# Kernel tuning notes

Measured on AMD Instinct MI355X. Metric: run time of the kernel, lower is better.

## Reference

```python
import jax, jax.numpy as jnp
import numpy as np

D_MODEL = 1024
NUM_HEADS = 16
DEPTH = D_MODEL // NUM_HEADS
MAX_LEN = 5000
B, S = 4, 1024


def _dense(x, W, b):
    return x @ W + b


def _split_heads(x, n_heads, depth):
    # [..., S, D] -> [..., H, S, depth]
    *lead, s, d = x.shape
    x = x.reshape(*lead, s, n_heads, depth)
    return jnp.swapaxes(x, -3, -2)


def setup_inputs() -> dict:
    key = jax.random.key(0)
    ks = jax.random.split(key, 12)
    w = 0.02  # glorot-ish scale to keep softmax logits sane
    inp = {
        'q': jax.random.normal(ks[0], (B, S, D_MODEL), jnp.float32),
        'k': jax.random.normal(ks[1], (B, S, D_MODEL), jnp.float32),
        'v': jax.random.normal(ks[2], (B, S, D_MODEL), jnp.float32),
        'Wq': jax.random.normal(ks[3], (D_MODEL, D_MODEL), jnp.float32) * w,
        'bq': jnp.zeros((D_MODEL,), jnp.float32),
        'Wk': jax.random.normal(ks[4], (D_MODEL, D_MODEL), jnp.float32) * w,
        'bk': jnp.zeros((D_MODEL,), jnp.float32),
        'Wv': jax.random.normal(ks[5], (D_MODEL, D_MODEL), jnp.float32) * w,
        'bv': jnp.zeros((D_MODEL,), jnp.float32),
        'Uq': jax.random.normal(ks[6], (D_MODEL, D_MODEL), jnp.float32) * w,
        'buq': jnp.zeros((D_MODEL,), jnp.float32),
        'Uk': jax.random.normal(ks[7], (D_MODEL, D_MODEL), jnp.float32) * w,
        'buk': jnp.zeros((D_MODEL,), jnp.float32),
        'pos_table': jax.random.normal(ks[8], (MAX_LEN, D_MODEL), jnp.float32) * w,
        'theta_cc': jnp.zeros((1, NUM_HEADS, 1, 1), jnp.float32),
        'theta_co': jnp.zeros((1, NUM_HEADS, 1, 1), jnp.float32),
        'theta_oc': jnp.zeros((1, NUM_HEADS, 1, 1), jnp.float32),
        'Wo': jax.random.normal(ks[9], (D_MODEL, D_MODEL), jnp.float32) * w,
        'bo': jnp.zeros((D_MODEL,), jnp.float32),
    }
    return inp


def reference(q, k, v, Wq, bq, Wk, bk, Wv, bv, Uq, buq, Uk, buk,
              pos_table, theta_cc, theta_co, theta_oc, Wo, bo):
    b, s, d = q.shape
    # content projections -> [B,H,S,depth]
    q_c = _split_heads(_dense(q, Wq, bq), NUM_HEADS, DEPTH)
    k_c = _split_heads(_dense(k, Wk, bk), NUM_HEADS, DEPTH)
    v_c = _split_heads(_dense(v, Wv, bv), NUM_HEADS, DEPTH)
    content_scores = jnp.einsum('bhqd,bhkd->bhqk', q_c, k_c)

    # untied positional scores (shared across batch): [1,H,S,S]
    pos_emb = pos_table[:s]                               # [S,D]
    q_p = _split_heads(_dense(pos_emb, Uq, buq)[None], NUM_HEADS, DEPTH)
    k_p = _split_heads(_dense(pos_emb, Uk, buk)[None], NUM_HEADS, DEPTH)
    pos_scores = jnp.einsum('bhqd,bhkd->bhqk', q_p, k_p)  # [1,H,S,S]

    # CLS-row/col overrides with learnable thetas
    pos_scores = pos_scores.at[:, :, 1:, 0:1].set(jnp.broadcast_to(theta_oc, (1, NUM_HEADS, s - 1, 1)))
    pos_scores = pos_scores.at[:, :, 0:1, 1:].set(jnp.broadcast_to(theta_co, (1, NUM_HEADS, 1, s - 1)))
    pos_scores = pos_scores.at[:, :, 0:1, 0:1].set(theta_cc)

    scores = (content_scores + pos_scores) / jnp.sqrt(jnp.float32(DEPTH))
    attn = jax.nn.softmax(scores, axis=-1)
    out = jnp.einsum('bhqk,bhkd->bhqd', attn, v_c)        # [B,H,S,depth]
    out = jnp.swapaxes(out, 1, 2).reshape(b, s, d)        # [B,S,D]
    return _dense(out, Wo, bo)
```

## Files before the change

kernel.cpp:

```cpp
#include <hip/hip_runtime.h>
#include <hip/hip_bf16.h>

typedef __hip_bfloat16 bf16;
typedef unsigned short u16;
typedef __attribute__((ext_vector_type(8))) short short8;
typedef __attribute__((ext_vector_type(4))) float f32x4;

#define D_MODEL 1024
#define NUM_HEADS 16
#define DEPTH 64
#define BATCH 4
#define SEQ 1024
#define BS (BATCH * SEQ)

__device__ __forceinline__ float ldDyn(const void* p, size_t i, int isbf) {
  return isbf ? __bfloat162float(((const bf16*)p)[i]) : ((const float*)p)[i];
}
__device__ __forceinline__ u16 f2bf(float f) {
  bf16 h = __float2bfloat16(f);
  return *(u16*)&h;
}
__device__ __forceinline__ void gl2lds16(const void* g, void* l) {
  __builtin_amdgcn_global_load_lds((const __attribute__((address_space(1))) unsigned int*)g,
                                   (__attribute__((address_space(3))) unsigned int*)l, 16, 0, 0);
}

__global__ void detect_kernel(const u16* __restrict__ q, int* __restrict__ flag) {
  if (threadIdx.x == 0 && blockIdx.x == 0) {
    int sane = 0;
    for (int i = 0; i < 64; ++i) {
      u16 h = q[2 * i];
      int e = (h >> 7) & 0xFF;
      if (e >= 100 && e <= 150) ++sane;
    }
    *flag = (sane >= 48) ? 1 : 0;
  }
}

__global__ __launch_bounds__(256) void convert_in(
    const void* __restrict__ q, const void* __restrict__ k, const void* __restrict__ v,
    const void* __restrict__ pos, u16* __restrict__ Qb, u16* __restrict__ Kb,
    u16* __restrict__ Vb, u16* __restrict__ Pb, const int* __restrict__ flagp) {
  const int isbf = *flagp;
  const int z = blockIdx.z;
  const void* src = (z == 0) ? q : (z == 1) ? k : (z == 2) ? v : pos;
  u16* dst = (z == 0) ? Qb : (z == 1) ? Kb : (z == 2) ? Vb : Pb;
  const size_t n8 = ((z == 3) ? (size_t)SEQ * D_MODEL : (size_t)BS * D_MODEL) / 8;
  for (size_t i = (size_t)blockIdx.x * 256 + threadIdx.x; i < n8; i += (size_t)gridDim.x * 256) {
    short8 o;
    if (isbf) {
      o = ((const short8*)src)[i];
    } else {
      const float4* f = (const float4*)src + 2 * i;
      float4 lo = f[0], hi = f[1];
      u16* pv = (u16*)&o;
      pv[0] = f2bf(lo.x); pv[1] = f2bf(lo.y); pv[2] = f2bf(lo.z); pv[3] = f2bf(lo.w);
      pv[4] = f2bf(hi.x); pv[5] = f2bf(hi.y); pv[6] = f2bf(hi.z); pv[7] = f2bf(hi.w);
    }
    ((short8*)dst)[i] = o;
  }
}

__global__ __launch_bounds__(256) void transpose_w(
    const void* W0, const void* W1, const void* W2, const void* W3, const void* W4,
    const void* W5, u16* __restrict__ WT, const int* __restrict__ flagp) {
  const int isbf = *flagp;
  const int z = blockIdx.z;
  const void* W = (z == 0) ? W0 : (z == 1) ? W1 : (z == 2) ? W2
                 : (z == 3) ? W3 : (z == 4) ? W4 : W5;
  u16* out = WT + (size_t)z * D_MODEL * D_MODEL;
  __shared__ u16 tile[32][33];
  const int t = threadIdx.x;
  const int tx = t & 31, ty = t >> 5;
  const int r0 = blockIdx.y * 32, c0 = blockIdx.x * 32;
#pragma unroll
  for (int i = 0; i < 4; ++i) {
    size_t gi = (size_t)(r0 + ty + 8 * i) * D_MODEL + c0 + tx;
    tile[ty + 8 * i][tx] = isbf ? ((const u16*)W)[gi] : f2bf(((const float*)W)[gi]);
  }
  __syncthreads();
#pragma unroll
  for (int i = 0; i < 4; ++i)
    out[(size_t)(c0 + ty + 8 * i) * D_MODEL + r0 + tx] = tile[tx][ty + 8 * i];
}

struct GArgs {
  const u16* A[5];
  const u16* W[5];
  const void* bias[5];
  void* C[5];
  int Mr[5];
  int om[5];
};

__global__ __launch_bounds__(256) void gemm_mfma(GArgs ga, const int* __restrict__ flagp) {
  const int isbf = *flagp;
  const int z = blockIdx.z;
  const int M = ga.Mr[z];
  const int lin = blockIdx.x + 8 * blockIdx.y;
  const int xcd = lin & 7;
  const int loc = lin >> 3;
  const int rowb = (loc & 3) * 8 + xcd;
  const int colb = loc >> 2;
  const int row0 = rowb * 128, col0 = colb * 128;
  if (row0 >= M) return;
  const u16* A = ga.A[z];
  const u16* WT = ga.W[z];
  const void* bias = ga.bias[z];
  void* C = ga.C[z];
  const int omode = ga.om[z];

  __shared__ short As[2][128][32];
  __shared__ short Bs[2][128][32];
  const int t = threadIdx.x;
  const int wave = t >> 6, lane = t & 63;
  const int quad = lane >> 4, c16 = lane & 15;
  const int wrow = wave >> 1, wcol = wave & 1;

  f32x4 acc[4][4];
#pragma unroll
  for (int mt = 0; mt < 4; ++mt)
#pragma unroll
    for (int nt = 0; nt < 4; ++nt) acc[mt][nt] = {0.f, 0.f, 0.f, 0.f};

#define G_STAGE(K0, BUF)                                                                  \
  {                                                                                       \
    _Pragma("unroll") for (int i = 0; i < 2; ++i) {                                       \
      int L = t + 256 * i;                                                                \
      int r = L >> 2;                                                                     \
      int kc = (L & 3) ^ ((r + (r >> 2)) & 3);                                            \
      gl2lds16(WT + (size_t)(col0 + r) * 1024 + (K0) + kc * 8,                            \
               (char*)&Bs[BUF][0][0] + (size_t)(i * 256 + wave * 64) * 16);               \
      gl2lds16(A + (size_t)(row0 + r) * 1024 + (K0) + kc * 8,                             \
               (char*)&As[BUF][0][0] + (size_t)(i * 256 + wave * 64) * 16);               \
    }                                                                                     \
  }

  G_STAGE(0, 0);
  __syncthreads();

  const int fsw = (c16 + (c16 >> 2)) & 3;

  for (int kk = 0; kk < 32; ++kk) {
    const int cur = kk & 1;
    if (kk < 31) G_STAGE((kk + 1) * 32, cur ^ 1);

    short8 af[4], bfv[4];
#pragma unroll
    for (int mt = 0; mt < 4; ++mt)
      af[mt] = *(const short8*)&As[cur][wrow * 64 + mt * 16 + c16][((quad ^ fsw) * 8)];
#pragma unroll
    for (int nt = 0; nt < 4; ++nt)
      bfv[nt] = *(const short8*)&Bs[cur][wcol * 64 + nt * 16 + c16][((quad ^ fsw) * 8)];
#pragma unroll
    for (int nt = 0; nt < 4; ++nt)
#pragma unroll
      for (int mt = 0; mt < 4; ++mt)
        acc[mt][nt] = __builtin_amdgcn_mfma_f32_16x16x32_bf16(af[mt], bfv[nt], acc[mt][nt], 0, 0, 0);

    __syncthreads();
  }
#undef G_STAGE

#pragma unroll
  for (int nt = 0; nt < 4; ++nt) {
    int gc = col0 + wcol * 64 + nt * 16 + c16;
    float bb = ldDyn(bias, gc, isbf);
#pragma unroll
    for (int mt = 0; mt < 4; ++mt) {
      int gr0 = row0 + wrow * 64 + mt * 16 + quad * 4;
      if (omode == 2) {
        __attribute__((ext_vector_type(4))) short pk;
#pragma unroll
        for (int r = 0; r < 4; ++r) pk[r] = (short)f2bf(acc[mt][nt][r] + bb);
        *(__attribute__((ext_vector_type(4))) short*)&((u16*)C)[(size_t)gc * M + gr0] = pk;
      } else if (omode == 1 || isbf) {
#pragma unroll
        for (int r = 0; r < 4; ++r)
          ((bf16*)C)[(size_t)(gr0 + r) * 1024 + gc] = __float2bfloat16(acc[mt][nt][r] + bb);
      } else {
#pragma unroll
        for (int r = 0; r < 4; ++r)
          ((float*)C)[(size_t)(gr0 + r) * 1024 + gc] = acc[mt][nt][r] + bb;
      }
    }
  }
}

__global__ __launch_bounds__(256) void flash_attn(
    const bf16* __restrict__ Qc, const bf16* __restrict__ Kc, const bf16* __restrict__ VcT,
    const bf16* __restrict__ Qp, const bf16* __restrict__ Kp,
    const void* __restrict__ th_cc, const void* __restrict__ th_co,
    const void* __restrict__ th_oc, bf16* __restrict__ O, const int* __restrict__ flagp) {
  const int isbf = *flagp;
  const int h = blockIdx.x, b = blockIdx.y, qt = blockIdx.z;
  const int t = threadIdx.x, wave = t >> 6, lane = t & 63;
  const int quad = lane >> 4, c16 = lane & 15;

  __shared__ short Kt[2][64][128];
  __shared__ short Vt[2][64][64];
  __shared__ short Pt[4][16][64];

  const float tcc = ldDyn(th_cc, h, isbf);
  const float tco = ldDyn(th_co, h, isbf);
  const float toc = ldDyn(th_oc, h, isbf);

  const bf16* kcb = Kc + (size_t)b * SEQ * 1024 + h * 64;
  const bf16* kpb = Kp + h * 64;
  const bf16* vtb = VcT + (size_t)(h * 64) * BS + (size_t)b * SEQ;

  const int rwK = lane >> 4, kcK = lane & 15;
  const int rwV = lane >> 3, kcV = lane & 7;

#define STAGE_K(KT2, BUF)                                                              \
  {                                                                                    \
    _Pragma("unroll") for (int i = 0; i < 4; ++i) {                                    \
      int r = wave * 16 + i * 4 + rwK;                                                 \
      int c = kcK ^ (r & 15);                                                          \
      int key = (KT2)*64 + r;                                                          \
      const bf16* src = (c < 8) ? kcb + (size_t)key * 1024 + c * 8                     \
                                : kpb + (size_t)key * 1024 + c * 8 - 64;               \
      gl2lds16(src, &Kt[BUF][wave * 16 + i * 4][0]);                                   \
    }                                                                                  \
  }
#define STAGE_V(KT2, BUF)                                                              \
  {                                                                                    \
    _Pragma("unroll") for (int j = 0; j < 2; ++j) {                                    \
      int d = wave * 16 + j * 8 + rwV;                                                 \
      int c = kcV ^ (d & 7);                                                           \
      gl2lds16(vtb + (size_t)d * BS + (KT2)*64 + c * 8, &Vt[BUF][wave * 16 + j * 8][0]); \
    }                                                                                  \
  }

  short8 qf[2][4];
#pragma unroll
  for (int mt = 0; mt < 2; ++mt) {
    int qrow = qt * 128 + wave * 32 + mt * 16 + c16;
#pragma unroll
    for (int ks = 0; ks < 4; ++ks) {
      int d = ks * 32 + quad * 8;
      const bf16* src = (d < 64) ? Qc + ((size_t)(b * SEQ + qrow)) * 1024 + h * 64 + d
                                 : Qp + (size_t)qrow * 1024 + h * 64 + (d - 64);
      qf[mt][ks] = *(const short8*)src;
    }
    if (qrow == 0) {
      qf[mt][2] = (short8)0;
      qf[mt][3] = (short8)0;
    }
  }

  f32x4 accO[2][4];
#pragma unroll
  for (int mt = 0; mt < 2; ++mt)
#pragma unroll
    for (int nt = 0; nt < 4; ++nt) accO[mt][nt] = {0.f, 0.f, 0.f, 0.f};
  float lrow[2][4] = {{0.f, 0.f, 0.f, 0.f}, {0.f, 0.f, 0.f, 0.f}};

  STAGE_K(0, 0);
  STAGE_V(0, 0);
  __syncthreads();
  if (t < 8) *(short8*)&Kt[0][0][64 + t * 8] = (short8)0;
  __syncthreads();

  for (int kt = 0; kt < 16; ++kt) {
    const int cur = kt & 1, nxt = cur ^ 1;
    if (kt < 15) {
      STAGE_K(kt + 1, nxt);
      STAGE_V(kt + 1, nxt);
    }

    f32x4 accS[2][4];
#pragma unroll
    for (int mt = 0; mt < 2; ++mt)
#pragma unroll
      for (int nt = 0; nt < 4; ++nt) accS[mt][nt] = {0.f, 0.f, 0.f, 0.f};
#pragma unroll
    for (int nt = 0; nt < 4; ++nt)
#pragma unroll
      for (int ks = 0; ks < 4; ++ks) {
        short8 kf = *(const short8*)&Kt[cur][nt * 16 + c16][((ks * 4 + quad) ^ c16) * 8];
#pragma unroll
        for (int mt = 0; mt < 2; ++mt)
          accS[mt][nt] = __builtin_amdgcn_mfma_f32_16x16x32_bf16(qf[mt][ks], kf, accS[mt][nt], 0, 0, 0);
      }

    short8 vbreg[2][4];
#pragma unroll
    for (int ks2 = 0; ks2 < 2; ++ks2)
#pragma unroll
      for (int nt = 0; nt < 4; ++nt)
        vbreg[ks2][nt] =
            *(const short8*)&Vt[cur][nt * 16 + c16][(((ks2 * 4 + quad) ^ (c16 & 7)) & 7) * 8];

#pragma unroll
    for (int mt = 0; mt < 2; ++mt) {
      float s[4][4];
#pragma unroll
      for (int nt = 0; nt < 4; ++nt)
#pragma unroll
        for (int r = 0; r < 4; ++r) s[nt][r] = accS[mt][nt][r] * 0.125f;

      if (kt == 0 || (qt == 0 && wave == 0 && mt == 0)) {
#pragma unroll
        for (int nt = 0; nt < 4; ++nt)
#pragma unroll
          for (int r = 0; r < 4; ++r) {
            int kcol = kt * 64 + nt * 16 + c16;
            int qrow = qt * 128 + wave * 32 + mt * 16 + quad * 4 + r;
            float add = 0.f;
            if (qrow == 0 && kcol == 0) add = tcc;
            else if (qrow == 0) add = tco;
            else if (kcol == 0) add = toc;
            s[nt][r] += add * 0.125f;
          }
      }
#pragma unroll
      for (int nt = 0; nt < 4; ++nt)
#pragma unroll
        for (int r = 0; r < 4; ++r) {
          float p = __expf(s[nt][r]);
          lrow[mt][r] += p;
          int row = quad * 4 + r;
          int ch = nt * 2 + (c16 >> 3);
          Pt[wave][row][((ch ^ (row & 7)) * 8) + (c16 & 7)] = (short)f2bf(p);
        }
#pragma unroll
      for (int ks2 = 0; ks2 < 2; ++ks2) {
        short8 pf = *(const short8*)&Pt[wave][c16][(((ks2 * 4 + quad) ^ (c16 & 7)) & 7) * 8];
#pragma unroll
        for (int nt = 0; nt < 4; ++nt)
          accO[mt][nt] = __builtin_amdgcn_mfma_f32_16x16x32_bf16(pf, vbreg[ks2][nt], accO[mt][nt], 0, 0, 0);
      }
    }
    __syncthreads();
  }

#pragma unroll
  for (int d = 1; d < 16; d <<= 1)
#pragma unroll
    for (int mt = 0; mt < 2; ++mt)
#pragma unroll
      for (int r = 0; r < 4; ++r) lrow[mt][r] += __shfl_xor(lrow[mt][r], d, 64);

#pragma unroll
  for (int mt = 0; mt < 2; ++mt)
#pragma unroll
    for (int nt = 0; nt < 4; ++nt)
#pragma unroll
      for (int r = 0; r < 4; ++r) {
        int qrow = qt * 128 + wave * 32 + mt * 16 + quad * 4 + r;
        O[((size_t)(b * SEQ + qrow)) * 1024 + h * 64 + nt * 16 + c16] =
            __float2bfloat16(accO[mt][nt][r] / lrow[mt][r]);
      }
#undef STAGE_K
#undef STAGE_V
}

extern "C" void kernel_launch(void* const* d_in, const int* in_sizes, int n_in,
                              void* d_out, int out_size, void* d_ws, size_t ws_size,
                              hipStream_t stream) {
  const void* q = d_in[0];
  const void* k = d_in[1];
  const void* v = d_in[2];
  const void* Wq = d_in[3];
  const void* bq = d_in[4];
  const void* Wk = d_in[5];
  const void* bk = d_in[6];
  const void* Wv = d_in[7];
  const void* bv = d_in[8];
  const void* Uq = d_in[9];
  const void* buq = d_in[10];
  const void* Uk = d_in[11];
  const void* buk = d_in[12];
  const void* pos = d_in[13];
  const void* th_cc = d_in[14];
  const void* th_co = d_in[15];
  const void* th_oc = d_in[16];
  const void* Wo = d_in[17];
  const void* bo = d_in[18];

  const int M = BS;
  const size_t DD = (size_t)D_MODEL * D_MODEL;
  char* wsb = (char*)d_ws;
  int* flag = (int*)wsb;
  bf16* Qc = (bf16*)(wsb + 256);
  bf16* Kc = Qc + (size_t)M * D_MODEL;
  bf16* VcT = Kc + (size_t)M * D_MODEL;
  bf16* Qp = VcT + (size_t)M * D_MODEL;
  bf16* Kp = Qp + (size_t)SEQ * D_MODEL;
  u16* WT = (u16*)(Kp + (size_t)SEQ * D_MODEL);
  bf16* AO = (bf16*)WT;
  u16* Qb = WT + 6 * DD;
  u16* Kb = Qb + (size_t)M * D_MODEL;
  u16* Vb = Kb + (size_t)M * D_MODEL;
  u16* Pb = Vb + (size_t)M * D_MODEL;

  detect_kernel<<<1, 64, 0, stream>>>((const u16*)q, flag);

  dim3 blk(256);
  convert_in<<<dim3(512, 1, 4), blk, 0, stream>>>(q, k, v, pos, Qb, Kb, Vb, Pb, flag);
  transpose_w<<<dim3(32, 32, 6), blk, 0, stream>>>(Wq, Wk, Wv, Uq, Uk, Wo, WT, flag);

  GArgs g1 = {{Qb, Kb, Vb, Pb, Pb},
              {WT + 0 * DD, WT + 1 * DD, WT + 2 * DD, WT + 3 * DD, WT + 4 * DD},
              {bq, bk, bv, buq, buk},
              {Qc, Kc, VcT, Qp, Kp},
              {M, M, M, SEQ, SEQ},
              {1, 1, 2, 1, 1}};
  gemm_mfma<<<dim3(8, 32, 5), blk, 0, stream>>>(g1, flag);

  flash_attn<<<dim3(NUM_HEADS, BATCH, SEQ / 128), blk, 0, stream>>>(
      Qc, Kc, VcT, Qp, Kp, th_cc, th_co, th_oc, AO, flag);

  GArgs g2 = {{(const u16*)AO, (const u16*)AO, (const u16*)AO, (const u16*)AO, (const u16*)AO},
              {WT + 5 * DD, WT + 5 * DD, WT + 5 * DD, WT + 5 * DD, WT + 5 * DD},
              {bo, bo, bo, bo, bo},
              {d_out, d_out, d_out, d_out, d_out},
              {M, M, M, M, M},
              {0, 0, 0, 0, 0}};
  gemm_mfma<<<dim3(8, 32, 1), blk, 0, stream>>>(g2, flag);
}
```

Baseline: 291.3 us.

## Triple-buffer GEMM K-loop with vmcnt waits and prioritize MFMA in attention

Converts the projection GEMM from a double-buffered loop with a full __syncthreads per K step to a three-stage ring buffer. It prefetches two stages ahead and uses s_waitcnt vmcnt(4) plus s_barrier, so only the oldest loads must have landed before compute starts. This is meant to hide global-to-LDS latency, at the cost of 50% more LDS per block; launch bounds now request 3 blocks per CU. Separately, the attention kernel raises wave priority around its MFMA sections with s_setprio so matrix work is scheduled ahead of other waves.

```diff
diff --git a/kernel.cpp b/kernel.cpp
--- a/kernel.cpp
+++ b/kernel.cpp
@@ -93,7 +93,7 @@
   int om[5];
 };
 
-__global__ __launch_bounds__(256) void gemm_mfma(GArgs ga, const int* __restrict__ flagp) {
+__global__ __launch_bounds__(256, 3) void gemm_mfma(GArgs ga, const int* __restrict__ flagp) {
   const int isbf = *flagp;
   const int z = blockIdx.z;
   const int M = ga.Mr[z];
@@ -110,8 +110,8 @@
   void* C = ga.C[z];
   const int omode = ga.om[z];
 
-  __shared__ short As[2][128][32];
-  __shared__ short Bs[2][128][32];
+  __shared__ short As[3][128][32];
+  __shared__ short Bs[3][128][32];
   const int t = threadIdx.x;
   const int wave = t >> 6, lane = t & 63;
   const int quad = lane >> 4, c16 = lane & 15;
@@ -136,31 +136,33 @@
     }                                                                                     \
   }
 
+  const int fsw = (c16 + (c16 >> 2)) & 3;
+
+#define COMPUTE(BUF)                                                                      \
+  {                                                                                       \
+    short8 af[4], bfv[4];                                                                 \
+    _Pragma("unroll") for (int mt = 0; mt < 4; ++mt)                                      \
+        af[mt] = *(const short8*)&As[BUF][wrow * 64 + mt * 16 + c16][((quad ^ fsw) * 8)]; \
+    _Pragma("unroll") for (int nt = 0; nt < 4; ++nt)                                      \
+        bfv[nt] = *(const short8*)&Bs[BUF][wcol * 64 + nt * 16 + c16][((quad ^ fsw) * 8)];\
+    _Pragma("unroll") for (int nt = 0; nt < 4; ++nt)                                      \
+      _Pragma("unroll") for (int mt = 0; mt < 4; ++mt)                                    \
+          acc[mt][nt] =                                                                   \
+              __builtin_amdgcn_mfma_f32_16x16x32_bf16(af[mt], bfv[nt], acc[mt][nt], 0, 0, 0); \
+  }
+
   G_STAGE(0, 0);
-  __syncthreads();
-
-  const int fsw = (c16 + (c16 >> 2)) & 3;
-
-  for (int kk = 0; kk < 32; ++kk) {
-    const int cur = kk & 1;
-    if (kk < 31) G_STAGE((kk + 1) * 32, cur ^ 1);
-
-    short8 af[4], bfv[4];
-#pragma unroll
-    for (int mt = 0; mt < 4; ++mt)
-      af[mt] = *(const short8*)&As[cur][wrow * 64 + mt * 16 + c16][((quad ^ fsw) * 8)];
-#pragma unroll
-    for (int nt = 0; nt < 4; ++nt)
-      bfv[nt] = *(const short8*)&Bs[cur][wcol * 64 + nt * 16 + c16][((quad ^ fsw) * 8)];
-#pragma unroll
-    for (int nt = 0; nt < 4; ++nt)
-#pragma unroll
-      for (int mt = 0; mt < 4; ++mt)
-        acc[mt][nt] = __builtin_amdgcn_mfma_f32_16x16x32_bf16(af[mt], bfv[nt], acc[mt][nt], 0, 0, 0);
-
-    __syncthreads();
-  }
+  G_STAGE(32, 1);
+#pragma unroll
+  for (int kk = 0; kk < 31; ++kk) {
+    asm volatile("s_waitcnt vmcnt(4)\n\ts_barrier" ::: "memory");
+    if (kk < 30) G_STAGE((kk + 2) * 32, (kk + 2) % 3);
+    COMPUTE(kk % 3);
+  }
+  asm volatile("s_waitcnt vmcnt(0)\n\ts_barrier" ::: "memory");
+  COMPUTE(1);
 #undef G_STAGE
+#undef COMPUTE
 
 #pragma unroll
   for (int nt = 0; nt < 4; ++nt) {
@@ -274,6 +276,7 @@
     for (int mt = 0; mt < 2; ++mt)
 #pragma unroll
       for (int nt = 0; nt < 4; ++nt) accS[mt][nt] = {0.f, 0.f, 0.f, 0.f};
+    __builtin_amdgcn_s_setprio(1);
 #pragma unroll
     for (int nt = 0; nt < 4; ++nt)
 #pragma unroll
@@ -283,6 +286,7 @@
         for (int mt = 0; mt < 2; ++mt)
           accS[mt][nt] = __builtin_amdgcn_mfma_f32_16x16x32_bf16(qf[mt][ks], kf, accS[mt][nt], 0, 0, 0);
       }
+    __builtin_amdgcn_s_setprio(0);
 
     short8 vbreg[2][4];
 #pragma unroll
@@ -324,6 +328,7 @@
           int ch = nt * 2 + (c16 >> 3);
           Pt[wave][row][((ch ^ (row & 7)) * 8) + (c16 & 7)] = (short)f2bf(p);
         }
+      __builtin_amdgcn_s_setprio(1);
 #pragma unroll
       for (int ks2 = 0; ks2 < 2; ++ks2) {
         short8 pf = *(const short8*)&Pt[wave][c16][(((ks2 * 4 + quad) ^ (c16 & 7)) & 7) * 8];
@@ -331,6 +336,7 @@
         for (int nt = 0; nt < 4; ++nt)
           accO[mt][nt] = __builtin_amdgcn_mfma_f32_16x16x32_bf16(pf, vbreg[ks2][nt], accO[mt][nt], 0, 0, 0);
       }
+      __builtin_amdgcn_s_setprio(0);
     }
     __syncthreads();
   }
```

After: 279.2 us. -4.2%, faster.
